# Kernel optimization log

Hardware: AMD Instinct MI355X
Metric: run time of the kernel (lower is better)

Reference implementation:

```python
import jax, jax.numpy as jnp
import numpy as np

EMPTY_IDX = 6  # relabeling of the original -1 ('EMPTY') expert to row 6 of the stacked tables


def setup_inputs() -> dict:
    key = jax.random.key(0)
    k1, k2, k3, k4, k5, k6 = jax.random.split(key, 6)
    B, L, H, T, E = 32, 2048, 768, 12, 7
    return {
        "sequence_output": jax.random.normal(k1, (B, L, H), dtype=jnp.float32),
        "module_net_w": jax.random.normal(k2, (E, H, H), dtype=jnp.float32),
        "span_net_w": jax.random.normal(k3, (E, H, 2), dtype=jnp.float32),
        "turns": jax.random.randint(k4, (B, T, 2), 0, L),
        "key_phrase_span": jax.random.randint(k5, (B, T, 2), 0, L),
        "module_index": jax.random.randint(k6, (B, T), 0, E),
    }


def reference(sequence_output, module_net_w, span_net_w, turns, key_phrase_span, module_index):
    seq = sequence_output            # [B, L, H]
    B, L, H = seq.shape
    T = turns.shape[1]
    f32 = seq.dtype

    eidx = module_index              # [B, T], 0..6 (6 == EMPTY, original -1)
    mod_mask = (eidx != EMPTY_IDX).astype(f32)            # module_index != -1
    start_pos = turns[:, :, 0]       # [B, T] turn start token positions
    turns_mask = (start_pos >= 0).astype(f32)             # turns[:,:,0] != -1

    # context_hidden_step = sequence_output[arange(B), start] for every step
    ctx = jnp.take_along_axis(seq, start_pos[:, :, None], axis=1)   # [B, T, H]

    # einsum('bh,bhz,blz->blz'): (ctx @ W_expert) broadcast-multiplied with seq.
    # Compute ctx @ W for ALL experts (tables are tiny), then gather per (b, t).
    cW_all = jnp.einsum('bth,ehz->btez', ctx, module_net_w)         # [B, T, 7, H]
    gidx = jnp.broadcast_to(eidx[:, :, None, None], (B, T, 1, H))
    cW = jnp.take_along_axis(cW_all, gidx, axis=2).squeeze(2)       # [B, T, H]

    span_w = span_net_w[eidx]        # [B, T, H, 2] per-sample expert span weights
    # logits[b,t,l,k] = sum_z seq[b,l,z] * cW[b,t,z] * span_w[b,t,z,k]
    v = cW[..., None] * span_w                                      # [B, T, H, 2]
    logits = jnp.einsum('blz,btzk->btlk', seq, v)                   # [B, T, L, 2]

    # CrossEntropyLoss(ignore_index=-1, reduction='none') over the L axis
    logsm = jax.nn.log_softmax(logits, axis=2)                      # [B, T, L, 2]
    tgt = key_phrase_span[:, :, :T][:, :T]  # [B, T, 2]
    tgt = key_phrase_span
    safe = jnp.clip(tgt, 0, L - 1)                                  # [B, T, 2]
    picked = jnp.take_along_axis(logsm, safe[:, :, None, :], axis=2).squeeze(2)  # [B, T, 2]
    ce = jnp.where(tgt >= 0, -picked, jnp.zeros((), f32))           # [B, T, 2]
    step_loss = 0.5 * (ce[..., 0] + ce[..., 1]) * mod_mask          # [B, T]

    loss = (step_loss * turns_mask).sum() / turns_mask.sum()
    return loss
```

## Files before the change

### kernel.cpp

```cpp
#include <hip/hip_runtime.h>
#include <math.h>

#define Bz 32
#define Lz 2048
#define Hz 768
#define Tz 12
#define Ez 7
#define EMPTYIDX 6
#define NCOL 24
#define LCHUNK 128
#define NCHUNK 16

#define K1A_ZC 3
#define K1A_HB 48
#define K1A_HC 16
__global__ void k1a_cw(const float* __restrict__ seq, const float* __restrict__ W,
                       const int* __restrict__ turns, const int* __restrict__ midx,
                       float* __restrict__ cW) {
    int bx = blockIdx.x;
    int e  = bx % Ez;
    int zc = (bx / Ez) % K1A_ZC;
    int hc = bx / (Ez * K1A_ZC);
    int z  = zc * 256 + threadIdx.x;
    int h0 = hc * K1A_HB;
    int tid = threadIdx.x;

    __shared__ int itemsS[Bz * Tz];
    __shared__ int cntS;
    if (tid == 0) cntS = 0;
    __syncthreads();
    for (int i = tid; i < Bz * Tz; i += 256) {
        int ei = midx[i];
        ei = min(max(ei, 0), Ez - 1);
        if (ei == e) {
            int p = atomicAdd(&cntS, 1);
            itemsS[p] = i;
        }
    }
    __syncthreads();
    int cnt = cntS;

    const float* Wb = W + ((size_t)e * Hz + h0) * Hz + z;
    float w[K1A_HB];
#pragma unroll
    for (int j = 0; j < K1A_HB; ++j) w[j] = Wb[(size_t)j * Hz];

    for (int n = 0; n < cnt; ++n) {
        int i  = itemsS[n];
        int b  = i / Tz;
        int st = turns[2 * i];
        st = min(max(st, 0), Lz - 1);
        const float* c = seq + ((size_t)(b * Lz + st)) * Hz + h0;
        float acc = 0.f;
#pragma unroll
        for (int j = 0; j < K1A_HB; ++j) acc = fmaf(c[j], w[j], acc);
        atomicAdd(&cW[(size_t)i * Hz + z], acc);
    }
}

__global__ void k1b_v(const float* __restrict__ cW, const float* __restrict__ spanw,
                      const int* __restrict__ midx, float* __restrict__ v) {
    int idx = blockIdx.x * 256 + threadIdx.x;
    int i = idx / Hz;
    int z = idx - i * Hz;
    int e = midx[i];
    e = min(max(e, 0), Ez - 1);
    float cw = cW[idx];
    int b = i / Tz, t = i - b * Tz;
    size_t vb = ((size_t)(b * NCOL + t * 2)) * Hz + z;
    v[vb]      = cw * spanw[(e * Hz + z) * 2 + 0];
    v[vb + Hz] = cw * spanw[(e * Hz + z) * 2 + 1];
}

#define BK 64
#define ATS (BK + 4)
__global__ void k2_logits(const float* __restrict__ seq, const float* __restrict__ v,
                          float* __restrict__ pm, float* __restrict__ ps) {
    int bx = blockIdx.x;
    int b  = bx / NCHUNK;
    int ch = bx % NCHUNK;
    int l0 = ch * LCHUNK;
    int tid = threadIdx.x;
    int rg = tid >> 3;
    int cg = tid & 7;
    __shared__ float at[LCHUNK][ATS];
    __shared__ float vt[NCOL][ATS];
    __shared__ float red_m[NCOL][33];
    __shared__ float red_s[NCOL][33];
    float acc[4][3];
#pragma unroll
    for (int r = 0; r < 4; ++r)
#pragma unroll
        for (int j = 0; j < 3; ++j) acc[r][j] = 0.f;

    const float* A = seq + ((size_t)b * Lz + l0) * Hz;
    const float* V = v + (size_t)b * NCOL * Hz;

    int ar = tid >> 4, ac4 = tid & 15;
    float4 ra[8];
    float4 rv0, rv1;
#pragma unroll
    for (int p = 0; p < 8; ++p) {
        int j = tid + p * 256, r = j >> 4, c4 = j & 15;
        ra[p] = *(const float4*)&A[(size_t)r * Hz + c4 * 4];
    }
    rv0 = *(const float4*)&V[(size_t)(tid >> 4) * Hz + (tid & 15) * 4];
    if (tid < 128) {
        int j = tid + 256;
        rv1 = *(const float4*)&V[(size_t)(j >> 4) * Hz + (j & 15) * 4];
    }

    for (int k0 = 0; k0 < Hz; k0 += BK) {
#pragma unroll
        for (int p = 0; p < 8; ++p) {
            int j = tid + p * 256, r = j >> 4, c4 = j & 15;
            *(float4*)&at[r][c4 * 4] = ra[p];
        }
        *(float4*)&vt[tid >> 4][(tid & 15) * 4] = rv0;
        if (tid < 128) {
            int j = tid + 256;
            *(float4*)&vt[j >> 4][(j & 15) * 4] = rv1;
        }
        __syncthreads();
        if (k0 + BK < Hz) {
#pragma unroll
            for (int p = 0; p < 8; ++p) {
                int j = tid + p * 256, r = j >> 4, c4 = j & 15;
                ra[p] = *(const float4*)&A[(size_t)r * Hz + k0 + BK + c4 * 4];
            }
            rv0 = *(const float4*)&V[(size_t)(tid >> 4) * Hz + k0 + BK + (tid & 15) * 4];
            if (tid < 128) {
                int j = tid + 256;
                rv1 = *(const float4*)&V[(size_t)(j >> 4) * Hz + k0 + BK + (j & 15) * 4];
            }
        }
#pragma unroll
        for (int kk = 0; kk < BK; kk += 4) {
            float4 a0 = *(const float4*)&at[rg +  0][kk];
            float4 a1 = *(const float4*)&at[rg + 32][kk];
            float4 a2 = *(const float4*)&at[rg + 64][kk];
            float4 a3 = *(const float4*)&at[rg + 96][kk];
            float4 v0 = *(const float4*)&vt[cg * 3 + 0][kk];
            float4 v1 = *(const float4*)&vt[cg * 3 + 1][kk];
            float4 v2 = *(const float4*)&vt[cg * 3 + 2][kk];
#define DOT(ACC, AV, VV) ACC = fmaf(AV.w, VV.w, fmaf(AV.z, VV.z, fmaf(AV.y, VV.y, fmaf(AV.x, VV.x, ACC))))
            DOT(acc[0][0], a0, v0); DOT(acc[0][1], a0, v1); DOT(acc[0][2], a0, v2);
            DOT(acc[1][0], a1, v0); DOT(acc[1][1], a1, v1); DOT(acc[1][2], a1, v2);
            DOT(acc[2][0], a2, v0); DOT(acc[2][1], a2, v1); DOT(acc[2][2], a2, v2);
            DOT(acc[3][0], a3, v0); DOT(acc[3][1], a3, v1); DOT(acc[3][2], a3, v2);
#undef DOT
        }
        __syncthreads();
    }
    (void)ar; (void)ac4;
#pragma unroll
    for (int j = 0; j < 3; ++j) {
        int c = cg * 3 + j;
        float m = fmaxf(fmaxf(acc[0][j], acc[1][j]), fmaxf(acc[2][j], acc[3][j]));
        float s = expf(acc[0][j] - m) + expf(acc[1][j] - m) +
                  expf(acc[2][j] - m) + expf(acc[3][j] - m);
        red_m[c][rg] = m;
        red_s[c][rg] = s;
    }
    __syncthreads();
    if (tid < NCOL) {
        int c = tid;
        float m = red_m[c][0];
        for (int r = 1; r < 32; ++r) m = fmaxf(m, red_m[c][r]);
        float s = 0.f;
        for (int r = 0; r < 32; ++r) s += red_s[c][r] * expf(red_m[c][r] - m);
        pm[((size_t)b * NCOL + c) * NCHUNK + ch] = m;
        ps[((size_t)b * NCOL + c) * NCHUNK + ch] = s;
    }
}

__global__ void k3_picked(const float* __restrict__ seq, const float* __restrict__ v,
                          const int* __restrict__ kps, float* __restrict__ picked) {
    int i = blockIdx.x;
    int b = i / Tz, t = i % Tz;
    int lane = threadIdx.x;
    for (int k = 0; k < 2; ++k) {
        int tgt  = kps[2 * i + k];
        int safe = min(max(tgt, 0), Lz - 1);
        const float* srow = seq + ((size_t)b * Lz + safe) * Hz;
        const float* vcol = v + ((size_t)(b * NCOL + t * 2 + k)) * Hz;
        float sum = 0.f;
#pragma unroll
        for (int q = 0; q < Hz / 64; ++q) {
            int z = lane + q * 64;
            sum = fmaf(srow[z], vcol[z], sum);
        }
        for (int o = 32; o > 0; o >>= 1) sum += __shfl_down(sum, o, 64);
        if (lane == 0) picked[b * NCOL + t * 2 + k] = sum;
    }
}

__global__ void k4_final(const int* __restrict__ midx, const int* __restrict__ turns,
                         const int* __restrict__ kps,
                         const float* __restrict__ pm, const float* __restrict__ ps,
                         const float* __restrict__ picked, float* __restrict__ out) {
    int tid = threadIdx.x;
    int i = tid;
    int b = i / Tz, t = i % Tz;
    int e = midx[i];
    float modm  = (e != EMPTYIDX) ? 1.f : 0.f;
    float tmask = (turns[2 * i] >= 0) ? 1.f : 0.f;
    float ce[2];
#pragma unroll
    for (int k = 0; k < 2; ++k) {
        int c = t * 2 + k;
        const float* pmr = pm + ((size_t)b * NCOL + c) * NCHUNK;
        const float* psr = ps + ((size_t)b * NCOL + c) * NCHUNK;
        float m = pmr[0];
        for (int chn = 1; chn < NCHUNK; ++chn) m = fmaxf(m, pmr[chn]);
        float s = 0.f;
        for (int chn = 0; chn < NCHUNK; ++chn) s += psr[chn] * expf(pmr[chn] - m);
        float lse = m + logf(s);
        int tgt = kps[2 * i + k];
        ce[k] = (tgt >= 0) ? (lse - picked[b * NCOL + c]) : 0.f;
    }
    float contrib = 0.5f * (ce[0] + ce[1]) * modm * tmask;

    __shared__ float wsum[6], wmask[6];
    float sl = contrib, sm = tmask;
    for (int o = 32; o > 0; o >>= 1) {
        sl += __shfl_down(sl, o, 64);
        sm += __shfl_down(sm, o, 64);
    }
    int w = tid >> 6, lane = tid & 63;
    if (lane == 0) { wsum[w] = sl; wmask[w] = sm; }
    __syncthreads();
    if (tid == 0) {
        float a = 0.f, mk = 0.f;
        for (int ww = 0; ww < 6; ++ww) { a += wsum[ww]; mk += wmask[ww]; }
        out[0] = a / mk;
    }
}

extern "C" void kernel_launch(void* const* d_in, const int* in_sizes, int n_in,
                              void* d_out, int out_size, void* d_ws, size_t ws_size,
                              hipStream_t stream) {
    const float* seq   = (const float*)d_in[0];
    const float* W     = (const float*)d_in[1];
    const float* spanw = (const float*)d_in[2];
    const int*   turns = (const int*)d_in[3];
    const int*   kps   = (const int*)d_in[4];
    const int*   midx  = (const int*)d_in[5];
    float* out = (float*)d_out;

    char* ws = (char*)d_ws;
    float* cW     = (float*)(ws + 0);
    float* v      = (float*)(ws + 1179648);
    float* pm     = (float*)(ws + 1179648 + 2359296);
    float* ps     = (float*)(ws + 1179648 + 2359296 + 49152);
    float* picked = (float*)(ws + 1179648 + 2359296 + 98304);

    hipMemsetAsync(cW, 0, (size_t)384 * Hz * sizeof(float), stream);
    hipLaunchKernelGGL(k1a_cw, dim3(Ez * K1A_ZC * K1A_HC), dim3(256), 0, stream,
                       seq, W, turns, midx, cW);
    hipLaunchKernelGGL(k1b_v, dim3((384 * Hz) / 256), dim3(256), 0, stream,
                       cW, spanw, midx, v);
    hipLaunchKernelGGL(k2_logits, dim3(Bz * NCHUNK), dim3(256), 0, stream, seq, v, pm, ps);
    hipLaunchKernelGGL(k3_picked, dim3(Bz * Tz), dim3(64), 0, stream, seq, v, kps, picked);
    hipLaunchKernelGGL(k4_final, dim3(1), dim3(Bz * Tz), 0, stream,
                       midx, turns, kps, pm, ps, picked, out);
}
```

Measured before the change: 428.6 us.

## Compute logits with bf16 MFMA in small single-wave blocks and fold picked-logit extraction

The FP32 FMA logits GEMM is replaced by a bf16 MFMA kernel (16x16x32) running one wavefront per 32-row chunk, for 2048 blocks. Operands are converted to bf16 with round-to-nearest while being staged in LDS. The separate picked-logit kernel is removed, and its values are taken from the MFMA accumulators. This reduces compute cost and drops one launch plus its redundant seq reads, but lowers precision to bf16 and removes register prefetch double buffering.

```diff
diff --git a/kernel.cpp b/kernel.cpp
--- a/kernel.cpp
+++ b/kernel.cpp
@@ -8,8 +8,11 @@
 #define Ez 7
 #define EMPTYIDX 6
 #define NCOL 24
-#define LCHUNK 128
-#define NCHUNK 16
+#define RPB 32
+#define NCH 64
+
+typedef float f32x4 __attribute__((ext_vector_type(4)));
+typedef short s16x8 __attribute__((ext_vector_type(8)));
 
 #define K1A_ZC 3
 #define K1A_HB 48
@@ -72,126 +75,119 @@
     v[vb + Hz] = cw * spanw[(e * Hz + z) * 2 + 1];
 }
 
-#define BK 64
-#define ATS (BK + 4)
-__global__ void k2_logits(const float* __restrict__ seq, const float* __restrict__ v,
-                          float* __restrict__ pm, float* __restrict__ ps) {
-    int bx = blockIdx.x;
-    int b  = bx / NCHUNK;
-    int ch = bx % NCHUNK;
-    int l0 = ch * LCHUNK;
-    int tid = threadIdx.x;
-    int rg = tid >> 3;
-    int cg = tid & 7;
-    __shared__ float at[LCHUNK][ATS];
-    __shared__ float vt[NCOL][ATS];
-    __shared__ float red_m[NCOL][33];
-    __shared__ float red_s[NCOL][33];
-    float acc[4][3];
-#pragma unroll
-    for (int r = 0; r < 4; ++r)
-#pragma unroll
-        for (int j = 0; j < 3; ++j) acc[r][j] = 0.f;
+__device__ __forceinline__ unsigned int pk2(float x, float y) {
+    unsigned int a = __float_as_uint(x), b = __float_as_uint(y);
+    a = a + 0x7FFFu + ((a >> 16) & 1u);
+    b = b + 0x7FFFu + ((b >> 16) & 1u);
+    return (a >> 16) | (b & 0xFFFF0000u);
+}
+
+__global__ void __launch_bounds__(64, 2)
+k2_mfma(const float* __restrict__ seq, const float* __restrict__ v,
+        const int* __restrict__ kps,
+        float* __restrict__ pm, float* __restrict__ ps,
+        float* __restrict__ picked) {
+    int bx   = blockIdx.x;
+    int b    = bx >> 6;
+    int ch   = bx & (NCH - 1);
+    int l0   = ch * RPB;
+    int lane = threadIdx.x;
+    int n16  = lane & 15, quad = lane >> 4;
+
+    __shared__ unsigned int lds_u[2560];
+
+    {
+        int base = 1280 + 24 * 40 + lane * 5;
+#pragma unroll
+        for (int j = 0; j < 5; ++j) lds_u[base + j] = 0;
+    }
 
     const float* A = seq + ((size_t)b * Lz + l0) * Hz;
     const float* V = v + (size_t)b * NCOL * Hz;
 
-    int ar = tid >> 4, ac4 = tid & 15;
-    float4 ra[8];
-    float4 rv0, rv1;
-#pragma unroll
-    for (int p = 0; p < 8; ++p) {
-        int j = tid + p * 256, r = j >> 4, c4 = j & 15;
-        ra[p] = *(const float4*)&A[(size_t)r * Hz + c4 * 4];
-    }
-    rv0 = *(const float4*)&V[(size_t)(tid >> 4) * Hz + (tid & 15) * 4];
-    if (tid < 128) {
-        int j = tid + 256;
-        rv1 = *(const float4*)&V[(size_t)(j >> 4) * Hz + (j & 15) * 4];
-    }
-
-    for (int k0 = 0; k0 < Hz; k0 += BK) {
+    f32x4 acc[2][2];
+#pragma unroll
+    for (int mt = 0; mt < 2; ++mt)
+#pragma unroll
+        for (int nt = 0; nt < 2; ++nt) acc[mt][nt] = (f32x4){0.f, 0.f, 0.f, 0.f};
+
+    for (int kt = 0; kt < 12; ++kt) {
+        int k0 = kt * 64;
+        float4 ra[8], rv[6];
 #pragma unroll
         for (int p = 0; p < 8; ++p) {
-            int j = tid + p * 256, r = j >> 4, c4 = j & 15;
-            *(float4*)&at[r][c4 * 4] = ra[p];
-        }
-        *(float4*)&vt[tid >> 4][(tid & 15) * 4] = rv0;
-        if (tid < 128) {
-            int j = tid + 256;
-            *(float4*)&vt[j >> 4][(j & 15) * 4] = rv1;
+            int c = p * 64 + lane, r = c >> 4, qc = c & 15;
+            ra[p] = *(const float4*)&A[(size_t)r * Hz + k0 + qc * 4];
+        }
+#pragma unroll
+        for (int p = 0; p < 6; ++p) {
+            int c = p * 64 + lane, r = c >> 4, qc = c & 15;
+            rv[p] = *(const float4*)&V[(size_t)r * Hz + k0 + qc * 4];
         }
         __syncthreads();
-        if (k0 + BK < Hz) {
-#pragma unroll
-            for (int p = 0; p < 8; ++p) {
-                int j = tid + p * 256, r = j >> 4, c4 = j & 15;
-                ra[p] = *(const float4*)&A[(size_t)r * Hz + k0 + BK + c4 * 4];
+#pragma unroll
+        for (int p = 0; p < 8; ++p) {
+            int c = p * 64 + lane, r = c >> 4, qc = c & 15;
+            uint2 w; w.x = pk2(ra[p].x, ra[p].y); w.y = pk2(ra[p].z, ra[p].w);
+            *(uint2*)&lds_u[r * 40 + qc * 2] = w;
+        }
+#pragma unroll
+        for (int p = 0; p < 6; ++p) {
+            int c = p * 64 + lane, r = c >> 4, qc = c & 15;
+            uint2 w; w.x = pk2(rv[p].x, rv[p].y); w.y = pk2(rv[p].z, rv[p].w);
+            *(uint2*)&lds_u[1280 + r * 40 + qc * 2] = w;
+        }
+        __syncthreads();
+#pragma unroll
+        for (int s = 0; s < 2; ++s) {
+            s16x8 af0 = *(const s16x8*)&lds_u[(0 * 16 + n16) * 40 + (s * 4 + quad) * 4];
+            s16x8 af1 = *(const s16x8*)&lds_u[(1 * 16 + n16) * 40 + (s * 4 + quad) * 4];
+            s16x8 bf0 = *(const s16x8*)&lds_u[1280 + (0 * 16 + n16) * 40 + (s * 4 + quad) * 4];
+            s16x8 bf1 = *(const s16x8*)&lds_u[1280 + (1 * 16 + n16) * 40 + (s * 4 + quad) * 4];
+            acc[0][0] = __builtin_amdgcn_mfma_f32_16x16x32_bf16(af0, bf0, acc[0][0], 0, 0, 0);
+            acc[0][1] = __builtin_amdgcn_mfma_f32_16x16x32_bf16(af0, bf1, acc[0][1], 0, 0, 0);
+            acc[1][0] = __builtin_amdgcn_mfma_f32_16x16x32_bf16(af1, bf0, acc[1][0], 0, 0, 0);
+            acc[1][1] = __builtin_amdgcn_mfma_f32_16x16x32_bf16(af1, bf1, acc[1][1], 0, 0, 0);
+        }
+    }
+
+#pragma unroll
+    for (int nt = 0; nt < 2; ++nt) {
+        f32x4 u0 = acc[0][nt], u1 = acc[1][nt];
+        float m = fmaxf(fmaxf(fmaxf(u0.x, u0.y), fmaxf(u0.z, u0.w)),
+                        fmaxf(fmaxf(u1.x, u1.y), fmaxf(u1.z, u1.w)));
+        float s = expf(u0.x - m) + expf(u0.y - m) + expf(u0.z - m) + expf(u0.w - m)
+                + expf(u1.x - m) + expf(u1.y - m) + expf(u1.z - m) + expf(u1.w - m);
+#pragma unroll
+        for (int mask = 16; mask <= 32; mask += 16) {
+            float om = __shfl_xor(m, mask, 64);
+            float os = __shfl_xor(s, mask, 64);
+            float nm = fmaxf(m, om);
+            s = s * expf(m - nm) + os * expf(om - nm);
+            m = nm;
+        }
+        int c = nt * 16 + n16;
+        if (quad == 0 && c < NCOL) {
+            pm[((size_t)b * NCOL + c) * NCH + ch] = m;
+            ps[((size_t)b * NCOL + c) * NCH + ch] = s;
+        }
+    }
+
+#pragma unroll
+    for (int c = 0; c < NCOL; ++c) {
+        int t = c >> 1, kk = c & 1;
+        int tgt = kps[(b * Tz + t) * 2 + kk];
+        int safe = min(max(tgt, 0), Lz - 1);
+        if ((safe >> 5) == ch) {
+            int lr = safe & 31;
+            int nt = c >> 4, n16c = c & 15;
+            int mt = lr >> 4, qo = (lr >> 2) & 3, rg = lr & 3;
+            if (lane == qo * 16 + n16c) {
+                f32x4 a4 = mt ? acc[1][nt] : acc[0][nt];
+                float val = (rg == 0) ? a4.x : (rg == 1) ? a4.y : (rg == 2) ? a4.z : a4.w;
+                picked[b * NCOL + c] = val;
             }
-            rv0 = *(const float4*)&V[(size_t)(tid >> 4) * Hz + k0 + BK + (tid & 15) * 4];
-            if (tid < 128) {
-                int j = tid + 256;
-                rv1 = *(const float4*)&V[(size_t)(j >> 4) * Hz + k0 + BK + (j & 15) * 4];
-            }
-        }
-#pragma unroll
-        for (int kk = 0; kk < BK; kk += 4) {
-            float4 a0 = *(const float4*)&at[rg +  0][kk];
-            float4 a1 = *(const float4*)&at[rg + 32][kk];
-            float4 a2 = *(const float4*)&at[rg + 64][kk];
-            float4 a3 = *(const float4*)&at[rg + 96][kk];
-            float4 v0 = *(const float4*)&vt[cg * 3 + 0][kk];
-            float4 v1 = *(const float4*)&vt[cg * 3 + 1][kk];
-            float4 v2 = *(const float4*)&vt[cg * 3 + 2][kk];
-#define DOT(ACC, AV, VV) ACC = fmaf(AV.w, VV.w, fmaf(AV.z, VV.z, fmaf(AV.y, VV.y, fmaf(AV.x, VV.x, ACC))))
-            DOT(acc[0][0], a0, v0); DOT(acc[0][1], a0, v1); DOT(acc[0][2], a0, v2);
-            DOT(acc[1][0], a1, v0); DOT(acc[1][1], a1, v1); DOT(acc[1][2], a1, v2);
-            DOT(acc[2][0], a2, v0); DOT(acc[2][1], a2, v1); DOT(acc[2][2], a2, v2);
-            DOT(acc[3][0], a3, v0); DOT(acc[3][1], a3, v1); DOT(acc[3][2], a3, v2);
-#undef DOT
-        }
-        __syncthreads();
-    }
-    (void)ar; (void)ac4;
-#pragma unroll
-    for (int j = 0; j < 3; ++j) {
-        int c = cg * 3 + j;
-        float m = fmaxf(fmaxf(acc[0][j], acc[1][j]), fmaxf(acc[2][j], acc[3][j]));
-        float s = expf(acc[0][j] - m) + expf(acc[1][j] - m) +
-                  expf(acc[2][j] - m) + expf(acc[3][j] - m);
-        red_m[c][rg] = m;
-        red_s[c][rg] = s;
-    }
-    __syncthreads();
-    if (tid < NCOL) {
-        int c = tid;
-        float m = red_m[c][0];
-        for (int r = 1; r < 32; ++r) m = fmaxf(m, red_m[c][r]);
-        float s = 0.f;
-        for (int r = 0; r < 32; ++r) s += red_s[c][r] * expf(red_m[c][r] - m);
-        pm[((size_t)b * NCOL + c) * NCHUNK + ch] = m;
-        ps[((size_t)b * NCOL + c) * NCHUNK + ch] = s;
-    }
-}
-
-__global__ void k3_picked(const float* __restrict__ seq, const float* __restrict__ v,
-                          const int* __restrict__ kps, float* __restrict__ picked) {
-    int i = blockIdx.x;
-    int b = i / Tz, t = i % Tz;
-    int lane = threadIdx.x;
-    for (int k = 0; k < 2; ++k) {
-        int tgt  = kps[2 * i + k];
-        int safe = min(max(tgt, 0), Lz - 1);
-        const float* srow = seq + ((size_t)b * Lz + safe) * Hz;
-        const float* vcol = v + ((size_t)(b * NCOL + t * 2 + k)) * Hz;
-        float sum = 0.f;
-#pragma unroll
-        for (int q = 0; q < Hz / 64; ++q) {
-            int z = lane + q * 64;
-            sum = fmaf(srow[z], vcol[z], sum);
-        }
-        for (int o = 32; o > 0; o >>= 1) sum += __shfl_down(sum, o, 64);
-        if (lane == 0) picked[b * NCOL + t * 2 + k] = sum;
+        }
     }
 }
 
@@ -209,12 +205,12 @@
 #pragma unroll
     for (int k = 0; k < 2; ++k) {
         int c = t * 2 + k;
-        const float* pmr = pm + ((size_t)b * NCOL + c) * NCHUNK;
-        const float* psr = ps + ((size_t)b * NCOL + c) * NCHUNK;
+        const float* pmr = pm + ((size_t)b * NCOL + c) * NCH;
+        const float* psr = ps + ((size_t)b * NCOL + c) * NCH;
         float m = pmr[0];
-        for (int chn = 1; chn < NCHUNK; ++chn) m = fmaxf(m, pmr[chn]);
+        for (int chn = 1; chn < NCH; ++chn) m = fmaxf(m, pmr[chn]);
         float s = 0.f;
-        for (int chn = 0; chn < NCHUNK; ++chn) s += psr[chn] * expf(pmr[chn] - m);
+        for (int chn = 0; chn < NCH; ++chn) s += psr[chn] * expf(pmr[chn] - m);
         float lse = m + logf(s);
         int tgt = kps[2 * i + k];
         ce[k] = (tgt >= 0) ? (lse - picked[b * NCOL + c]) : 0.f;
@@ -251,17 +247,17 @@
     char* ws = (char*)d_ws;
     float* cW     = (float*)(ws + 0);
     float* v      = (float*)(ws + 1179648);
-    float* pm     = (float*)(ws + 1179648 + 2359296);
-    float* ps     = (float*)(ws + 1179648 + 2359296 + 49152);
-    float* picked = (float*)(ws + 1179648 + 2359296 + 98304);
+    float* pm     = (float*)(ws + 3538944);
+    float* ps     = (float*)(ws + 3735552);
+    float* picked = (float*)(ws + 3932160);
 
     hipMemsetAsync(cW, 0, (size_t)384 * Hz * sizeof(float), stream);
     hipLaunchKernelGGL(k1a_cw, dim3(Ez * K1A_ZC * K1A_HC), dim3(256), 0, stream,
                        seq, W, turns, midx, cW);
     hipLaunchKernelGGL(k1b_v, dim3((384 * Hz) / 256), dim3(256), 0, stream,
                        cW, spanw, midx, v);
-    hipLaunchKernelGGL(k2_logits, dim3(Bz * NCHUNK), dim3(256), 0, stream, seq, v, pm, ps);
-    hipLaunchKernelGGL(k3_picked, dim3(Bz * Tz), dim3(64), 0, stream, seq, v, kps, picked);
+    hipLaunchKernelGGL(k2_mfma, dim3(Bz * NCH), dim3(64), 0, stream,
+                       seq, v, kps, pm, ps, picked);
     hipLaunchKernelGGL(k4_final, dim3(1), dim3(Bz * Tz), 0, stream,
                        midx, turns, kps, pm, ps, picked, out);
 }
```

Result: faster. 382.0 us (-10.9%).
